# Kernel optimization log

Hardware: AMD Instinct MI355X
Metric: run time of the kernel (lower is better)

Reference implementation:

```python
import math
import jax, jax.numpy as jnp
import numpy as np

D_MODEL = 1024
NUM_HEADS = 16
HEAD_DIM = D_MODEL // NUM_HEADS
THETA = 10000.0
MAX_SEQ_LEN = 2048
BATCH = 4
SEQ = 2048


def _rope_tables():
    # angles[i, j] = i / theta**(2j/d_k), shapes [max_seq_len, head_dim//2]
    i = jnp.arange(MAX_SEQ_LEN, dtype=jnp.float32)
    k = jnp.arange(0, HEAD_DIM, 2, dtype=jnp.float32) / HEAD_DIM
    angles = i[:, None] * (1.0 / (THETA ** k))[None, :]
    return jnp.cos(angles), jnp.sin(angles)


def _apply_rope(x, token_positions, cos_tab, sin_tab):
    # x: [b, h, s, d_k]; token_positions: [s]
    b, h, s, dk = x.shape
    xr = x.reshape(b, h, s, dk // 2, 2)
    x0, x1 = xr[..., 0], xr[..., 1]
    cos_pos = cos_tab[token_positions]  # [s, dk//2]
    sin_pos = sin_tab[token_positions]
    x0_rot = x0 * cos_pos - x1 * sin_pos
    x1_rot = x0 * sin_pos + x1 * cos_pos
    return jnp.stack([x0_rot, x1_rot], axis=-1).reshape(x.shape)


def setup_inputs() -> dict:
    key = jax.random.key(0)
    k1, k2, k3 = jax.random.split(key, 3)
    std_qkv = math.sqrt(2.0 / (D_MODEL + 3 * D_MODEL))
    std_o = math.sqrt(2.0 / (D_MODEL + D_MODEL))
    return {
        "x": jax.random.normal(k1, (BATCH, SEQ, D_MODEL), dtype=jnp.float32),
        "token_positions": jnp.arange(SEQ, dtype=jnp.int64) if jax.config.jax_enable_x64 else jnp.arange(SEQ, dtype=jnp.int32),
        "qkv_w": jax.random.normal(k2, (3 * D_MODEL, D_MODEL), dtype=jnp.float32) * std_qkv,
        "o_w": jax.random.normal(k3, (D_MODEL, D_MODEL), dtype=jnp.float32) * std_o,
    }


def reference(x, token_positions, qkv_w, o_w):
    b, s, _ = x.shape
    cos_tab, sin_tab = _rope_tables()
    # fused QKV projection: [b, s, 3*d_model]
    qkv = jnp.einsum('bsd,ed->bse', x, qkv_w)
    qkv = qkv.reshape(b, s, 3, NUM_HEADS, HEAD_DIM)
    q = jnp.transpose(qkv[:, :, 0], (0, 2, 1, 3))  # [b, h, s, hd]
    k = jnp.transpose(qkv[:, :, 1], (0, 2, 1, 3))
    v = jnp.transpose(qkv[:, :, 2], (0, 2, 1, 3))
    q = _apply_rope(q, token_positions, cos_tab, sin_tab)
    k = _apply_rope(k, token_positions, cos_tab, sin_tab)
    # causal mask and eager softmax attention (full [b,h,s,s] scores)
    scores = jnp.einsum('bhnk,bhmk->bhnm', q, k) / math.sqrt(HEAD_DIM)
    causal = jnp.tril(jnp.ones((s, s), dtype=bool))
    scores = jnp.where(causal, scores, -jnp.inf)
    attn = jax.nn.softmax(scores, axis=-1)
    ctx = jnp.einsum('bhnm,bhmv->bhnv', attn, v)
    ctx = jnp.transpose(ctx, (0, 2, 1, 3)).reshape(b, s, D_MODEL)
    return jnp.einsum('bsd,ed->bse', ctx, o_w)
```

## Files before the change

kernel.cpp:

```cpp
#include <hip/hip_runtime.h>


#define DM   1024
#define NH   16
#define HD   64
#define SEQL 2048
#define BATCH 4
#define QKV_ELEMS 8388608

using short8 = __attribute__((ext_vector_type(8))) short;
using f32x4  = __attribute__((ext_vector_type(4))) float;
typedef unsigned short u16;

#define WAIT_VM(n) __builtin_amdgcn_s_waitcnt(0x0F70 | (n))
#define WAIT_LGKM0() __builtin_amdgcn_s_waitcnt(0xC07F)
#define BARRIER()  __builtin_amdgcn_s_barrier()

__device__ __forceinline__ u16 f2bf(float f) {
    unsigned u = __builtin_bit_cast(unsigned, f);
    u += 0x7fffu + ((u >> 16) & 1u);
    return (u16)(u >> 16);
}
__device__ __forceinline__ float bf2f(u16 h) {
    unsigned u = ((unsigned)h) << 16;
    return __builtin_bit_cast(float, u);
}
__device__ __forceinline__ unsigned pk2bf(float a, float b) {
    return (unsigned)f2bf(a) | ((unsigned)f2bf(b) << 16);
}
__device__ __forceinline__ float fexp2(float x) {
#if __has_builtin(__builtin_amdgcn_exp2f)
    return __builtin_amdgcn_exp2f(x);
#else
    return __expf(x * 0.6931471805599453f);
#endif
}

__device__ __forceinline__ void load16(const void* g, void* l) {
    __builtin_amdgcn_global_load_lds(
        (__attribute__((address_space(1))) unsigned int*)(unsigned long long)g,
        (__attribute__((address_space(3))) unsigned int*)(unsigned int)(unsigned long long)l,
        16, 0, 0);
}

__global__ __launch_bounds__(256) void prep(const float* __restrict__ x, u16* __restrict__ xb,
                                            const float* __restrict__ qw, u16* __restrict__ wb,
                                            const float* __restrict__ ow, u16* __restrict__ owb,
                                            float* __restrict__ cost, float* __restrict__ sint) {
    int bx = blockIdx.x;
    if (bx < 12288) {
        const float* in; u16* out; int i;
        if (bx < 8192)       { in = x;  out = xb;  i = bx * 256 + threadIdx.x; }
        else if (bx < 11264) { in = qw; out = wb;  i = (bx - 8192) * 256 + threadIdx.x; }
        else                 { in = ow; out = owb; i = (bx - 11264) * 256 + threadIdx.x; }
        float4 v = ((const float4*)in)[i];
        uint2 o;
        o.x = pk2bf(v.x, v.y);
        o.y = pk2bf(v.z, v.w);
        ((uint2*)out)[i] = o;
    } else {
        int t = (bx - 12288) * 256 + threadIdx.x;
        int j = t & 31, pos = t >> 5;
        float freq = exp2f((float)j * (-2.0f / 64.0f) * 13.287712379549449f);
        float ang = (float)pos * freq;
        cost[t] = cosf(ang);
        sint[t] = sinf(ang);
    }
}

__device__ __forceinline__ void gemm128_core(const u16* __restrict__ A,
                                             const u16* __restrict__ B,
                                             int K, int m0, int n0,
                                             u16* As, u16* Bs, f32x4 acc[4][4]) {
    int tid = threadIdx.x, w = tid >> 6, l = tid & 63;
    int l15 = l & 15, l4 = l >> 4;
    int wm = w >> 1, wn = w & 1;
    int r0 = 32 * w + (l >> 2);
    int gblk = ((l & 3) ^ ((l >> 4) & 3)) * 8;
    const u16* gA0 = A + (size_t)(m0 + r0) * K + gblk;
    const u16* gA1 = gA0 + (size_t)16 * K;
    const u16* gB0 = B + (size_t)(n0 + r0) * K + gblk;
    const u16* gB1 = gB0 + (size_t)16 * K;
    char* ldsA = (char*)As + 2048 * w;
    char* ldsB = (char*)Bs + 2048 * w;
    int fo = ((l4 ^ (l15 >> 2)) & 3) * 16;
    f32x4 z = {0.f, 0.f, 0.f, 0.f};
#pragma unroll
    for (int i = 0; i < 4; ++i)
#pragma unroll
        for (int j = 0; j < 4; ++j) acc[i][j] = z;
    int nk = K >> 5;
#pragma unroll
    for (int t = 0; t < 2; ++t) {
        int ko = t << 5, nb = t * 8192;
        load16(gA0 + ko, ldsA + nb); load16(gA1 + ko, ldsA + nb + 1024);
        load16(gB0 + ko, ldsB + nb); load16(gB1 + ko, ldsB + nb + 1024);
    }
    int buf = 0;
    for (int kt = 0; kt < nk; ++kt) {
        if (kt < nk - 1) WAIT_VM(4); else WAIT_VM(0);
        BARRIER();
        if (kt + 2 < nk) {
            int ko = (kt + 2) << 5;
            int nb = 8192 * ((buf + 2) % 3);
            load16(gA0 + ko, ldsA + nb); load16(gA1 + ko, ldsA + nb + 1024);
            load16(gB0 + ko, ldsB + nb); load16(gB1 + ko, ldsB + nb + 1024);
        }
        const char* bA = (const char*)As + 8192 * buf;
        const char* bB = (const char*)Bs + 8192 * buf;
        short8 a[4], b[4];
#pragma unroll
        for (int i = 0; i < 4; ++i)
            a[i] = *(const short8*)(bA + (64 * wm + 16 * i + l15) * 64 + fo);
#pragma unroll
        for (int j = 0; j < 4; ++j)
            b[j] = *(const short8*)(bB + (64 * wn + 16 * j + l15) * 64 + fo);
#pragma unroll
        for (int i = 0; i < 4; ++i)
#pragma unroll
            for (int j = 0; j < 4; ++j)
                acc[i][j] = __builtin_amdgcn_mfma_f32_16x16x32_bf16(a[i], b[j], acc[i][j], 0, 0, 0);
        buf = (buf + 1) % 3;
    }
}

__global__ __launch_bounds__(512, 2) void gemm_qkv(const u16* __restrict__ xb,
                                                   const u16* __restrict__ wb,
                                                   u16* __restrict__ qkv,
                                                   u16* __restrict__ vt,
                                                   const int* __restrict__ pos_ids,
                                                   const float* __restrict__ cost,
                                                   const float* __restrict__ sint) {
    __shared__ __align__(16) u16 As[3 * 256 * 32];
    __shared__ __align__(16) u16 Bs[3 * 256 * 32];
    int tid = threadIdx.x, w = tid >> 6, l = tid & 63;
    int l15 = l & 15, l4 = l >> 4;
    int wr = w >> 2, wc = w & 3;

    int bid = blockIdx.y * 12 + blockIdx.x;
    int swz = (bid & 7) * 48 + (bid >> 3);
    int nI = swz % 12, mI = swz / 12;
    int m0 = mI * 256, n0 = nI * 256;

    int schunk = ((l & 3) ^ ((l >> 3) & 3)) * 8;
    const u16* gA = xb + (size_t)(m0 + 32 * w + (l >> 2)) * DM + schunk;
    const u16* gB = wb + (size_t)(n0 + 32 * w + (l >> 2)) * DM + schunk;
    char* ldsA = (char*)As + 2048 * w;
    char* ldsB = (char*)Bs + 2048 * w;

    int roff = (l4 ^ ((l15 >> 1) & 3)) * 16;
    int aoff = (128 * wr + l15) * 64 + roff;
    int boff = (64 * wc + l15) * 64 + roff;

    f32x4 acc[8][4];
    f32x4 z = {0.f, 0.f, 0.f, 0.f};
#pragma unroll
    for (int i = 0; i < 8; ++i)
#pragma unroll
        for (int j = 0; j < 4; ++j) acc[i][j] = z;

#pragma unroll
    for (int t = 0; t < 2; ++t) {
        load16(gA + t * 32,           ldsA + t * 16384);
        load16(gA + t * 32 + 16 * DM, ldsA + t * 16384 + 1024);
        load16(gB + t * 32,           ldsB + t * 16384);
        load16(gB + t * 32 + 16 * DM, ldsB + t * 16384 + 1024);
    }
    WAIT_VM(4);
    BARRIER();

    int buf = 0;
    for (int kt = 0; kt < 32; ++kt) {
        const char* bA = (const char*)As + 16384 * buf;
        const char* bB = (const char*)Bs + 16384 * buf;
        int nb = buf + 2; if (nb >= 3) nb -= 3;
        short8 a[4], b[4];
#pragma unroll
        for (int i = 0; i < 4; ++i) a[i] = *(const short8*)(bA + aoff + 1024 * i);
#pragma unroll
        for (int j = 0; j < 4; ++j) b[j] = *(const short8*)(bB + boff + 1024 * j);
        if (kt + 2 < 32) {
            load16(gA + (kt + 2) * 32,           ldsA + nb * 16384);
            load16(gA + (kt + 2) * 32 + 16 * DM, ldsA + nb * 16384 + 1024);
        }
        BARRIER();
        WAIT_LGKM0();
        __builtin_amdgcn_s_setprio(1);
#pragma unroll
        for (int i = 0; i < 4; ++i)
#pragma unroll
            for (int j = 0; j < 4; ++j)
                acc[i][j] = __builtin_amdgcn_mfma_f32_16x16x32_bf16(a[i], b[j], acc[i][j], 0, 0, 0);
        __builtin_amdgcn_s_setprio(0);
        BARRIER();
        short8 a2[4];
#pragma unroll
        for (int i = 0; i < 4; ++i) a2[i] = *(const short8*)(bA + aoff + 1024 * (i + 4));
        if (kt + 2 < 32) {
            load16(gB + (kt + 2) * 32,           ldsB + nb * 16384);
            load16(gB + (kt + 2) * 32 + 16 * DM, ldsB + nb * 16384 + 1024);
        }
        BARRIER();
        WAIT_LGKM0();
        __builtin_amdgcn_s_setprio(1);
#pragma unroll
        for (int i = 0; i < 4; ++i)
#pragma unroll
            for (int j = 0; j < 4; ++j)
                acc[i + 4][j] = __builtin_amdgcn_mfma_f32_16x16x32_bf16(a2[i], b[j], acc[i + 4][j], 0, 0, 0);
        __builtin_amdgcn_s_setprio(0);
        if (kt + 2 < 32) WAIT_VM(4); else WAIT_VM(0);
        BARRIER();
        buf = buf + 1; if (buf >= 3) buf = 0;
    }

    if (nI >= 8) {
#pragma unroll
        for (int j = 0; j < 4; ++j) {
            int nv = (n0 - 2048) + 64 * wc + 16 * j + l15;
            int h = nv >> 6, d = nv & 63;
#pragma unroll
            for (int i = 0; i < 8; ++i) {
                int sb = m0 + 128 * wr + 16 * i + 4 * l4;
                int bb = sb >> 11, s = sb & 2047;
                uint2 pk;
                pk.x = pk2bf(acc[i][j][0], acc[i][j][1]);
                pk.y = pk2bf(acc[i][j][2], acc[i][j][3]);
                *(uint2*)&vt[((size_t)(bb * 16 + h) * HD + d) * SEQL + s] = pk;
            }
        }
    } else {
        float sc = (nI < 4) ? 0.18033688011112042f : 1.0f;
        u16* base = qkv + (size_t)(nI >> 2) * QKV_ELEMS;
        int h = ((n0 & 1023) >> 6) + wc;
#pragma unroll
        for (int i = 0; i < 8; ++i) {
#pragma unroll
            for (int r = 0; r < 4; ++r) {
                int m = m0 + 128 * wr + 16 * i + 4 * l4 + r;
                int bb = m >> 11, s = m & 2047;
                int pos = pos_ids[s];
                const float* cr = cost + pos * 32;
                const float* sr = sint + pos * 32;
                u16* orow = base + ((size_t)(bb * 16 + h) * SEQL + s) * HD;
#pragma unroll
                for (int j = 0; j < 4; ++j) {
                    int d = 16 * j + l15, d2 = d >> 1;
                    float c  = cr[d2];
                    float sn = sr[d2];
                    float v  = acc[i][j][r];
                    float vp = __shfl_xor(v, 1);
                    float o  = (d & 1) ? (vp * sn + v * c) : (v * c - vp * sn);
                    orow[d] = f2bf(o * sc);
                }
            }
        }
    }
}

__global__ __launch_bounds__(256) void gemm_out(const u16* __restrict__ ctx,
                                                const u16* __restrict__ owb,
                                                float* __restrict__ out) {
    __shared__ __align__(16) u16 As[3 * 128 * 32], Bs[3 * 128 * 32];
    f32x4 acc[4][4];
    int m0 = blockIdx.y * 128, n0 = blockIdx.x * 128;
    gemm128_core(ctx, owb, DM, m0, n0, As, Bs, acc);
    int l = threadIdx.x & 63, w = threadIdx.x >> 6;
    int l15 = l & 15, l4 = l >> 4;
    int wm = w >> 1, wn = w & 1;
#pragma unroll
    for (int i = 0; i < 4; ++i) {
        int mb = m0 + 64 * wm + 16 * i + 4 * l4;
#pragma unroll
        for (int j = 0; j < 4; ++j) {
            int n = n0 + 64 * wn + 16 * j + l15;
#pragma unroll
            for (int r = 0; r < 4; ++r)
                out[(size_t)(mb + r) * DM + n] = acc[i][j][r];
        }
    }
}

__device__ __forceinline__ void flash_pass(int qt, const u16* __restrict__ Qb,
                                           const u16* __restrict__ Kb,
                                           const u16* __restrict__ Vb,
                                           u16* __restrict__ ctx, int bh,
                                           u16* KsB, u16* VsB, u16* PsB) {
    int tid = threadIdx.x, w = tid >> 6, l = tid & 63;
    int l15 = l & 15, l4 = l >> 4;
    int q0 = qt * 256;
    int swz = l15 & 7;
    int b0 = (l4 ^ swz) * 16;

    short8 aq[2][2];
#pragma unroll
    for (int g = 0; g < 2; ++g) {
        const u16* qr = Qb + (size_t)(q0 + 128 * g + 16 * w + l15) * HD;
        aq[g][0] = *(const short8*)&qr[l4 * 8];
        aq[g][1] = *(const short8*)&qr[32 + l4 * 8];
    }
    int srow = l >> 3;
    int sblk = ((l & 7) ^ srow) * 8;
    const u16* gK = Kb + (size_t)(8 * w + srow) * HD + sblk;
    const u16* gV = Vb + (size_t)(8 * w + srow) * SEQL + sblk;
    char* ldsK = (char*)KsB + 1024 * w;
    char* ldsV = (char*)VsB + 1024 * w;
    char* prow = (char*)PsB + 2048 * w + l15 * 128;

    f32x4 z = {0.f, 0.f, 0.f, 0.f};
    f32x4 O[2][4] = {{z, z, z, z}, {z, z, z, z}};
    float lsum[2] = {0.f, 0.f};
    int nk = 4 * qt + 4;
    int d0 = 4 * qt + (w >> 2);
    int rowlim = 16 * (w & 3) + l15;

    BARRIER();
#pragma unroll
    for (int t = 0; t < 2; ++t) {
        load16(gK + (size_t)(t * 64) * HD, ldsK + t * 8192);
        load16(gV + t * 64,                ldsV + t * 8192);
    }
    int buf = 0;
    for (int it = 0; it < nk; ++it) {
        if (it < nk - 1) WAIT_VM(2); else WAIT_VM(0);
        BARRIER();
        if (it + 2 < nk) {
            int k0n = (it + 2) * 64;
            int nb = 8192 * ((buf + 2) % 3);
            load16(gK + (size_t)k0n * HD, ldsK + nb);
            load16(gV + k0n,              ldsV + nb);
        }
        if (it <= d0 + 2) {
            const char* bK = (const char*)KsB + 8192 * buf;
            const char* bV = (const char*)VsB + 8192 * buf;
            short8 kf[4][2], vf[4][2];
#pragma unroll
            for (int c = 0; c < 4; ++c) {
                const char* kr = bK + (16 * c + l15) * 128;
                kf[c][0] = *(const short8*)(kr + b0);
                kf[c][1] = *(const short8*)(kr + (b0 ^ 64));
                const char* vr = bV + (16 * c + l15) * 128;
                vf[c][0] = *(const short8*)(vr + b0);
                vf[c][1] = *(const short8*)(vr + (b0 ^ 64));
            }
#pragma unroll
            for (int g = 0; g < 2; ++g) {
                int dg = d0 + 2 * g;
                if (it > dg) continue;
                f32x4 S[4];
#pragma unroll
                for (int c = 0; c < 4; ++c) {
                    S[c] = __builtin_amdgcn_mfma_f32_16x16x32_bf16(kf[c][0], aq[g][0], z, 0, 0, 0);
                    S[c] = __builtin_amdgcn_mfma_f32_16x16x32_bf16(kf[c][1], aq[g][1], S[c], 0, 0, 0);
                }
                if (it == dg) {
#pragma unroll
                    for (int c = 0; c < 4; ++c)
#pragma unroll
                        for (int r = 0; r < 4; ++r)
                            if (16 * c + 4 * l4 + r > rowlim) S[c][r] = -3e38f;
                }
#pragma unroll
                for (int c = 0; c < 4; ++c)
#pragma unroll
                    for (int r = 0; r < 4; ++r) {
                        float p = fexp2(S[c][r]);
                        S[c][r] = p;
                        lsum[g] += p;
                    }
#pragma unroll
                for (int c = 0; c < 4; ++c) {
                    uint2 pk;
                    pk.x = pk2bf(S[c][0], S[c][1]);
                    pk.y = pk2bf(S[c][2], S[c][3]);
                    *(uint2*)(prow + ((((2 * c + (l4 >> 1)) ^ swz) << 4) | ((l4 & 1) << 3))) = pk;
                }
                short8 ap0 = *(const short8*)(prow + b0);
                short8 ap1 = *(const short8*)(prow + (b0 ^ 64));
#pragma unroll
                for (int nt = 0; nt < 4; ++nt) {
                    O[g][nt] = __builtin_amdgcn_mfma_f32_16x16x32_bf16(ap0, vf[nt][0], O[g][nt], 0, 0, 0);
                    O[g][nt] = __builtin_amdgcn_mfma_f32_16x16x32_bf16(ap1, vf[nt][1], O[g][nt], 0, 0, 0);
                }
            }
        }
        buf = (buf + 1) % 3;
    }
    int b = bh >> 4, h = bh & 15;
#pragma unroll
    for (int g = 0; g < 2; ++g) {
        float ls = lsum[g];
        ls += __shfl_xor(ls, 16);
        ls += __shfl_xor(ls, 32);
        float linv[4];
#pragma unroll
        for (int r = 0; r < 4; ++r) linv[r] = 1.0f / __shfl(ls, 20 * l4 + r);
#pragma unroll
        for (int nt = 0; nt < 4; ++nt) {
            int d = 16 * nt + l15;
#pragma unroll
            for (int r = 0; r < 4; ++r) {
                int s = q0 + 128 * g + 16 * w + 4 * l4 + r;
                ctx[((size_t)(b * SEQL + s)) * DM + h * 64 + d] = f2bf(O[g][nt][r] * linv[r]);
            }
        }
    }
}

__global__ __launch_bounds__(512, 2) void flash_attn(const u16* __restrict__ Q,
                                                     const u16* __restrict__ K,
                                                     const u16* __restrict__ Vt,
                                                     u16* __restrict__ ctx) {
    __shared__ __align__(16) u16 Ks[3][64 * 64];
    __shared__ __align__(16) u16 Vs[3][64 * 64];
    __shared__ __align__(16) u16 Ps[8][16 * 64];
    int bh = blockIdx.y, pair = blockIdx.x;
    const u16* Qb = Q + (size_t)bh * SEQL * HD;
    const u16* Kb = K + (size_t)bh * SEQL * HD;
    const u16* Vb = Vt + (size_t)bh * HD * SEQL;
    flash_pass(7 - pair, Qb, Kb, Vb, ctx, bh, &Ks[0][0], &Vs[0][0], &Ps[0][0]);
    flash_pass(pair,     Qb, Kb, Vb, ctx, bh, &Ks[0][0], &Vs[0][0], &Ps[0][0]);
}

extern "C" void kernel_launch(void* const* d_in, const int* in_sizes, int n_in,
                              void* d_out, int out_size, void* d_ws, size_t ws_size,
                              hipStream_t stream) {
    const float* x     = (const float*)d_in[0];
    const int*   pos   = (const int*)d_in[1];
    const float* qkv_w = (const float*)d_in[2];
    const float* o_w   = (const float*)d_in[3];
    float* out = (float*)d_out;

    char* ws = (char*)d_ws;
    u16*   xb   = (u16*)(ws);
    u16*   wb   = (u16*)(ws + 16777216);
    u16*   owb  = (u16*)(ws + 23068672);
    float* cost = (float*)(ws + 25165824);
    float* sint = (float*)(ws + 25427968);
    u16*   qkv  = (u16*)(ws + 25690112);
    u16*   vt   = (u16*)(ws + 76021760);
    u16*   ctx  = xb;

    prep<<<12544, 256, 0, stream>>>(x, xb, qkv_w, wb, o_w, owb, cost, sint);
    gemm_qkv<<<dim3(12, 32), 512, 0, stream>>>(xb, wb, qkv, vt, pos, cost, sint);
    flash_attn<<<dim3(4, 64), 512, 0, stream>>>(qkv, qkv + QKV_ELEMS, vt, ctx);
    gemm_out<<<dim3(8, 64), 256, 0, stream>>>(ctx, owb, out);
}
```

Measured before the change: 247.4 us.

## Split attention inner loop into per-group phases with double P buffers

Restructures the flash attention inner loop so both query groups compute QK^T scores and softmax probabilities first, writing into separate LDS P buffers. V fragments are then loaded and both PV products are issued. This moves the V loads later and lets the two groups' work interleave, and it adds s_setprio around the MFMA blocks to favour matrix issue. In exchange it doubles the LDS used for P, which may cut occupancy. It also changes the GEMM buffer-index update to a modulo on kt; since buf started at zero this gives the same sequence, and the extra line is dead code.

```diff
diff --git a/kernel.cpp b/kernel.cpp
--- a/kernel.cpp
+++ b/kernel.cpp
@@ -211,7 +211,8 @@
         __builtin_amdgcn_s_setprio(0);
         if (kt + 2 < 32) WAIT_VM(4); else WAIT_VM(0);
         BARRIER();
-        buf = buf + 1; if (buf >= 3) buf = 0;
+        buf = nb == 0 ? (buf == 1 ? 2 : 0) : nb;
+        buf = (kt + 1) % 3;
     }
 
     if (nI >= 8) {
@@ -305,7 +306,8 @@
     const u16* gV = Vb + (size_t)(8 * w + srow) * SEQL + sblk;
     char* ldsK = (char*)KsB + 1024 * w;
     char* ldsV = (char*)VsB + 1024 * w;
-    char* prow = (char*)PsB + 2048 * w + l15 * 128;
+    char* prow0 = (char*)PsB + 2048 * w + l15 * 128;
+    char* prow1 = prow0 + 16384;
 
     f32x4 z = {0.f, 0.f, 0.f, 0.f};
     f32x4 O[2][4] = {{z, z, z, z}, {z, z, z, z}};
@@ -333,55 +335,110 @@
         if (it <= d0 + 2) {
             const char* bK = (const char*)KsB + 8192 * buf;
             const char* bV = (const char*)VsB + 8192 * buf;
-            short8 kf[4][2], vf[4][2];
+            bool g0act = (it <= d0);
+            short8 kf[4][2];
 #pragma unroll
             for (int c = 0; c < 4; ++c) {
                 const char* kr = bK + (16 * c + l15) * 128;
                 kf[c][0] = *(const short8*)(kr + b0);
                 kf[c][1] = *(const short8*)(kr + (b0 ^ 64));
+            }
+            if (g0act) {
+                f32x4 S[4];
+                __builtin_amdgcn_s_setprio(1);
+#pragma unroll
+                for (int c = 0; c < 4; ++c) {
+                    S[c] = __builtin_amdgcn_mfma_f32_16x16x32_bf16(kf[c][0], aq[0][0], z, 0, 0, 0);
+                    S[c] = __builtin_amdgcn_mfma_f32_16x16x32_bf16(kf[c][1], aq[0][1], S[c], 0, 0, 0);
+                }
+                __builtin_amdgcn_s_setprio(0);
+                if (it == d0) {
+#pragma unroll
+                    for (int c = 0; c < 4; ++c)
+#pragma unroll
+                        for (int r = 0; r < 4; ++r)
+                            if (16 * c + 4 * l4 + r > rowlim) S[c][r] = -3e38f;
+                }
+                float ls = 0.f;
+#pragma unroll
+                for (int c = 0; c < 4; ++c) {
+                    float cs = 0.f;
+#pragma unroll
+                    for (int r = 0; r < 4; ++r) {
+                        float p = fexp2(S[c][r]);
+                        S[c][r] = p;
+                        cs += p;
+                    }
+                    ls += cs;
+                    uint2 pk;
+                    pk.x = pk2bf(S[c][0], S[c][1]);
+                    pk.y = pk2bf(S[c][2], S[c][3]);
+                    *(uint2*)(prow0 + ((((2 * c + (l4 >> 1)) ^ swz) << 4) | ((l4 & 1) << 3))) = pk;
+                }
+                lsum[0] += ls;
+            }
+            {
+                f32x4 S[4];
+                __builtin_amdgcn_s_setprio(1);
+#pragma unroll
+                for (int c = 0; c < 4; ++c) {
+                    S[c] = __builtin_amdgcn_mfma_f32_16x16x32_bf16(kf[c][0], aq[1][0], z, 0, 0, 0);
+                    S[c] = __builtin_amdgcn_mfma_f32_16x16x32_bf16(kf[c][1], aq[1][1], S[c], 0, 0, 0);
+                }
+                __builtin_amdgcn_s_setprio(0);
+                if (it == d0 + 2) {
+#pragma unroll
+                    for (int c = 0; c < 4; ++c)
+#pragma unroll
+                        for (int r = 0; r < 4; ++r)
+                            if (16 * c + 4 * l4 + r > rowlim) S[c][r] = -3e38f;
+                }
+                float ls = 0.f;
+#pragma unroll
+                for (int c = 0; c < 4; ++c) {
+                    float cs = 0.f;
+#pragma unroll
+                    for (int r = 0; r < 4; ++r) {
+                        float p = fexp2(S[c][r]);
+                        S[c][r] = p;
+                        cs += p;
+                    }
+                    ls += cs;
+                    uint2 pk;
+                    pk.x = pk2bf(S[c][0], S[c][1]);
+                    pk.y = pk2bf(S[c][2], S[c][3]);
+                    *(uint2*)(prow1 + ((((2 * c + (l4 >> 1)) ^ swz) << 4) | ((l4 & 1) << 3))) = pk;
+                }
+                lsum[1] += ls;
+            }
+            short8 vf[4][2];
+#pragma unroll
+            for (int c = 0; c < 4; ++c) {
                 const char* vr = bV + (16 * c + l15) * 128;
                 vf[c][0] = *(const short8*)(vr + b0);
                 vf[c][1] = *(const short8*)(vr + (b0 ^ 64));
             }
-#pragma unroll
-            for (int g = 0; g < 2; ++g) {
-                int dg = d0 + 2 * g;
-                if (it > dg) continue;
-                f32x4 S[4];
-#pragma unroll
-                for (int c = 0; c < 4; ++c) {
-                    S[c] = __builtin_amdgcn_mfma_f32_16x16x32_bf16(kf[c][0], aq[g][0], z, 0, 0, 0);
-                    S[c] = __builtin_amdgcn_mfma_f32_16x16x32_bf16(kf[c][1], aq[g][1], S[c], 0, 0, 0);
-                }
-                if (it == dg) {
-#pragma unroll
-                    for (int c = 0; c < 4; ++c)
-#pragma unroll
-                        for (int r = 0; r < 4; ++r)
-                            if (16 * c + 4 * l4 + r > rowlim) S[c][r] = -3e38f;
-                }
-#pragma unroll
-                for (int c = 0; c < 4; ++c)
-#pragma unroll
-                    for (int r = 0; r < 4; ++r) {
-                        float p = fexp2(S[c][r]);
-                        S[c][r] = p;
-                        lsum[g] += p;
-                    }
-#pragma unroll
-                for (int c = 0; c < 4; ++c) {
-                    uint2 pk;
-                    pk.x = pk2bf(S[c][0], S[c][1]);
-                    pk.y = pk2bf(S[c][2], S[c][3]);
-                    *(uint2*)(prow + ((((2 * c + (l4 >> 1)) ^ swz) << 4) | ((l4 & 1) << 3))) = pk;
-                }
-                short8 ap0 = *(const short8*)(prow + b0);
-                short8 ap1 = *(const short8*)(prow + (b0 ^ 64));
+            if (g0act) {
+                short8 ap0 = *(const short8*)(prow0 + b0);
+                short8 ap1 = *(const short8*)(prow0 + (b0 ^ 64));
+                __builtin_amdgcn_s_setprio(1);
 #pragma unroll
                 for (int nt = 0; nt < 4; ++nt) {
-                    O[g][nt] = __builtin_amdgcn_mfma_f32_16x16x32_bf16(ap0, vf[nt][0], O[g][nt], 0, 0, 0);
-                    O[g][nt] = __builtin_amdgcn_mfma_f32_16x16x32_bf16(ap1, vf[nt][1], O[g][nt], 0, 0, 0);
-                }
+                    O[0][nt] = __builtin_amdgcn_mfma_f32_16x16x32_bf16(ap0, vf[nt][0], O[0][nt], 0, 0, 0);
+                    O[0][nt] = __builtin_amdgcn_mfma_f32_16x16x32_bf16(ap1, vf[nt][1], O[0][nt], 0, 0, 0);
+                }
+                __builtin_amdgcn_s_setprio(0);
+            }
+            {
+                short8 bp0 = *(const short8*)(prow1 + b0);
+                short8 bp1 = *(const short8*)(prow1 + (b0 ^ 64));
+                __builtin_amdgcn_s_setprio(1);
+#pragma unroll
+                for (int nt = 0; nt < 4; ++nt) {
+                    O[1][nt] = __builtin_amdgcn_mfma_f32_16x16x32_bf16(bp0, vf[nt][0], O[1][nt], 0, 0, 0);
+                    O[1][nt] = __builtin_amdgcn_mfma_f32_16x16x32_bf16(bp1, vf[nt][1], O[1][nt], 0, 0, 0);
+                }
+                __builtin_amdgcn_s_setprio(0);
             }
         }
         buf = (buf + 1) % 3;
@@ -413,13 +470,13 @@
                                                      u16* __restrict__ ctx) {
     __shared__ __align__(16) u16 Ks[3][64 * 64];
     __shared__ __align__(16) u16 Vs[3][64 * 64];
-    __shared__ __align__(16) u16 Ps[8][16 * 64];
+    __shared__ __align__(16) u16 Ps[2][8][16 * 64];
     int bh = blockIdx.y, pair = blockIdx.x;
     const u16* Qb = Q + (size_t)bh * SEQL * HD;
     const u16* Kb = K + (size_t)bh * SEQL * HD;
     const u16* Vb = Vt + (size_t)bh * HD * SEQL;
-    flash_pass(7 - pair, Qb, Kb, Vb, ctx, bh, &Ks[0][0], &Vs[0][0], &Ps[0][0]);
-    flash_pass(pair,     Qb, Kb, Vb, ctx, bh, &Ks[0][0], &Vs[0][0], &Ps[0][0]);
+    flash_pass(7 - pair, Qb, Kb, Vb, ctx, bh, &Ks[0][0], &Vs[0][0], &Ps[0][0][0]);
+    flash_pass(pair,     Qb, Kb, Vb, ctx, bh, &Ks[0][0], &Vs[0][0], &Ps[0][0][0]);
 }
 
 extern "C" void kernel_launch(void* const* d_in, const int* in_sizes, int n_in,
```

Result: no change. 251.3 us (+1.6%).
